# Optimization experiments

Measured on AMD Instinct MI355X. Metric: run time of the kernel, lower is better.

The kernel has to match this reference:

```python
import jax, jax.numpy as jnp
import numpy as np

B, C, H1, W1 = 64, 3, 512, 512
H2, W2 = 224, 224


def setup_inputs() -> dict:
    key = jax.random.key(0)
    # images in [0,1] as produced by ToTensor / expected by ToPILImage
    x = jax.random.uniform(key, (B, C, H1, W1), dtype=jnp.float32)
    return {"input": x}


def reference(input) -> jnp.ndarray:
    # PIL Resize (default BILINEAR) performs an antialiased bilinear resize
    # when downsampling. jax.image.resize with method='bilinear' and
    # antialias=True matches this math, applied batched over [B, C].
    out_shape = (input.shape[0], input.shape[1], H2, W2)
    return jax.image.resize(input, out_shape, method="bilinear", antialias=True)
```

## Files before the change

kernel.cpp:

```cpp
#include <hip/hip_runtime.h>

#define IN_H 512
#define IN_W 512
#define OUT_H 224
#define OUT_W 224
#define OY 4
#define BLOCK 256


__global__ __launch_bounds__(BLOCK) void resize_aa_vfirst(
    const float* __restrict__ in, float* __restrict__ out) {

    __shared__ float s_v[OY][IN_W];
    __shared__ float s_wx[OUT_W][5];
    __shared__ int   s_ix0[OUT_W];

    const int bc  = blockIdx.x;
    const int oy0 = blockIdx.y * OY;
    const int tid = threadIdx.x;

    const float inv_scale = 16.f / 7.f;
    const float scl       = 7.f / 16.f;

    if (tid < OUT_W) {
        float cx  = (tid + 0.5f) * inv_scale - 0.5f;
        int   ix0 = (int)ceilf(cx - inv_scale);
        float w[5];
        float s = 0.f;
#pragma unroll
        for (int j = 0; j < 5; ++j) {
            int i = ix0 + j;
            float ww = 1.f - fabsf(cx - (float)i) * scl;
            ww = fmaxf(ww, 0.f);
            if (i < 0 || i >= IN_W) ww = 0.f;
            w[j] = ww;
            s += ww;
        }
        float invs = 1.f / s;
#pragma unroll
        for (int j = 0; j < 5; ++j) s_wx[tid][j] = w[j] * invs;
        s_ix0[tid] = ix0;
    }

    const float* src = in + (size_t)bc * (IN_H * IN_W);
    for (int q = tid; q < OY * (IN_W / 4); q += BLOCK) {
        int t  = q >> 7;
        int x0 = (q & 127) << 2;
        float cy  = (oy0 + t + 0.5f) * inv_scale - 0.5f;
        int   iy0 = (int)ceilf(cy - inv_scale);
        float4 acc = make_float4(0.f, 0.f, 0.f, 0.f);
        float s = 0.f;
#pragma unroll
        for (int j = 0; j < 5; ++j) {
            int i = iy0 + j;
            float ww = 1.f - fabsf(cy - (float)i) * scl;
            ww = fmaxf(ww, 0.f);
            if (i < 0 || i >= IN_H) ww = 0.f;
            s += ww;
            int r = min(max(i, 0), IN_H - 1);
            float4 v = *(const float4*)(src + (size_t)r * IN_W + x0);
            acc.x = fmaf(ww, v.x, acc.x);
            acc.y = fmaf(ww, v.y, acc.y);
            acc.z = fmaf(ww, v.z, acc.z);
            acc.w = fmaf(ww, v.w, acc.w);
        }
        float invs = 1.f / s;
        acc.x *= invs; acc.y *= invs; acc.z *= invs; acc.w *= invs;
        *(float4*)(&s_v[t][x0]) = acc;
    }

    __syncthreads();

    for (int idx = tid; idx < OY * OUT_W; idx += BLOCK) {
        int t  = idx / OUT_W;
        int ox = idx - t * OUT_W;
        int ix0 = s_ix0[ox];
        float acc = 0.f;
#pragma unroll
        for (int j = 0; j < 5; ++j) {
            int c = min(max(ix0 + j, 0), IN_W - 1);
            acc = fmaf(s_wx[ox][j], s_v[t][c], acc);
        }
        out[((size_t)bc * OUT_H + (oy0 + t)) * OUT_W + ox] = acc;
    }
}

extern "C" void kernel_launch(void* const* d_in, const int* in_sizes, int n_in,
                              void* d_out, int out_size, void* d_ws, size_t ws_size,
                              hipStream_t stream) {
    const float* in = (const float*)d_in[0];
    float* out = (float*)d_out;
    dim3 block(BLOCK);
    dim3 grid(64 * 3, OUT_H / OY);
    hipLaunchKernelGGL(resize_aa_vfirst, grid, block, 0, stream, in, out);
}
```

Baseline: 282.8 us.

## Double output rows per block, precompute vertical weights, and remap blocks for XCD locality

Each workgroup now produces 8 output rows instead of 4, which halves the number of blocks and reduces how often overlapping input rows are re-read. Vertical filter weights and start indices are computed once per block into shared memory, so the per-element weight math drops out of the vertical pass, at the cost of one extra barrier. A 1D grid is remapped so consecutive tiles of the same image land on the same XCD (bid&7 interleave), which is meant to improve L2 reuse of the shared input rows. Larger shared memory per block may reduce occupancy.

```diff
diff --git a/kernel.cpp b/kernel.cpp
--- a/kernel.cpp
+++ b/kernel.cpp
@@ -4,8 +4,11 @@
 #define IN_W 512
 #define OUT_H 224
 #define OUT_W 224
-#define OY 4
+#define OY 8
 #define BLOCK 256
+#define NTILE (OUT_H / OY)
+#define NIMG  (64 * 3)
+#define NWG   (NIMG * NTILE)
 
 
 __global__ __launch_bounds__(BLOCK) void resize_aa_vfirst(
@@ -14,9 +17,14 @@
     __shared__ float s_v[OY][IN_W];
     __shared__ float s_wx[OUT_W][5];
     __shared__ int   s_ix0[OUT_W];
+    __shared__ float s_wy[OY][5];
+    __shared__ int   s_iy0[OY];
 
-    const int bc  = blockIdx.x;
-    const int oy0 = blockIdx.y * OY;
+    int bid  = blockIdx.x;
+    int wg   = (bid & 7) * (NWG / 8) + (bid >> 3);
+    int img  = wg / NTILE;
+    int tile = wg - img * NTILE;
+    const int oy0 = tile * OY;
     const int tid = threadIdx.x;
 
     const float inv_scale = 16.f / 7.f;
@@ -40,15 +48,11 @@
 #pragma unroll
         for (int j = 0; j < 5; ++j) s_wx[tid][j] = w[j] * invs;
         s_ix0[tid] = ix0;
-    }
-
-    const float* src = in + (size_t)bc * (IN_H * IN_W);
-    for (int q = tid; q < OY * (IN_W / 4); q += BLOCK) {
-        int t  = q >> 7;
-        int x0 = (q & 127) << 2;
+    } else if (tid >= 240 && tid < 240 + OY) {
+        int   t   = tid - 240;
         float cy  = (oy0 + t + 0.5f) * inv_scale - 0.5f;
         int   iy0 = (int)ceilf(cy - inv_scale);
-        float4 acc = make_float4(0.f, 0.f, 0.f, 0.f);
+        float w[5];
         float s = 0.f;
 #pragma unroll
         for (int j = 0; j < 5; ++j) {
@@ -56,16 +60,35 @@
             float ww = 1.f - fabsf(cy - (float)i) * scl;
             ww = fmaxf(ww, 0.f);
             if (i < 0 || i >= IN_H) ww = 0.f;
+            w[j] = ww;
             s += ww;
-            int r = min(max(i, 0), IN_H - 1);
+        }
+        float invs = 1.f / s;
+#pragma unroll
+        for (int j = 0; j < 5; ++j) s_wy[t][j] = w[j] * invs;
+        s_iy0[t] = iy0;
+    }
+
+    __syncthreads();
+
+    const float* src = in + (size_t)img * (IN_H * IN_W);
+#pragma unroll
+    for (int k = 0; k < OY * (IN_W / 4) / BLOCK; ++k) {
+        int q  = tid + k * BLOCK;
+        int t  = q >> 7;
+        int x0 = (q & 127) << 2;
+        int iy0 = s_iy0[t];
+        float4 acc = make_float4(0.f, 0.f, 0.f, 0.f);
+#pragma unroll
+        for (int j = 0; j < 5; ++j) {
+            float ww = s_wy[t][j];
+            int r = min(max(iy0 + j, 0), IN_H - 1);
             float4 v = *(const float4*)(src + (size_t)r * IN_W + x0);
             acc.x = fmaf(ww, v.x, acc.x);
             acc.y = fmaf(ww, v.y, acc.y);
             acc.z = fmaf(ww, v.z, acc.z);
             acc.w = fmaf(ww, v.w, acc.w);
         }
-        float invs = 1.f / s;
-        acc.x *= invs; acc.y *= invs; acc.z *= invs; acc.w *= invs;
         *(float4*)(&s_v[t][x0]) = acc;
     }
 
@@ -81,7 +104,7 @@
             int c = min(max(ix0 + j, 0), IN_W - 1);
             acc = fmaf(s_wx[ox][j], s_v[t][c], acc);
         }
-        out[((size_t)bc * OUT_H + (oy0 + t)) * OUT_W + ox] = acc;
+        out[((size_t)img * OUT_H + (oy0 + t)) * OUT_W + ox] = acc;
     }
 }
 
@@ -91,6 +114,6 @@
     const float* in = (const float*)d_in[0];
     float* out = (float*)d_out;
     dim3 block(BLOCK);
-    dim3 grid(64 * 3, OUT_H / OY);
+    dim3 grid(NWG);
     hipLaunchKernelGGL(resize_aa_vfirst, grid, block, 0, stream, in, out);
 }
```

Result: no change. 284.1 us (+0.4%).
